# Optimization experiments

Hardware: AMD Instinct MI355X
Metric: run time of the kernel (lower is better)

Reference implementation:

```python
import jax, jax.numpy as jnp
import numpy as np

N_NODES = 100000   # n_all_trajs
N_EDGES = 640000
HIDDEN = 128
N_USERS = 1000


def gcn_conv(x, edge_index, edge_weight, W, b, num_nodes):
    """PyG GCNConv with add_self_loops=False, normalize=True.
    out[col] += (deg^-1/2[row] * w * deg^-1/2[col]) * (x @ W)[row]; then + b.
    deg is weighted in-degree at the target (col) nodes."""
    row, col = edge_index[0], edge_index[1]
    deg = jax.ops.segment_sum(edge_weight, col, num_segments=num_nodes)
    deg_inv_sqrt = jnp.where(deg > 0, jax.lax.rsqrt(jnp.maximum(deg, 1e-30)), 0.0)
    norm = deg_inv_sqrt[row] * edge_weight * deg_inv_sqrt[col]   # [E]
    h = x @ W                                                    # [N, H]
    msg = h[row] * norm[:, None]                                 # [E, H] gather+scale
    out = jax.ops.segment_sum(msg, col, num_segments=num_nodes)  # scatter-add
    return out + b


def setup_inputs() -> dict:
    key = jax.random.key(0)
    ks = jax.random.split(key, 9)
    edge_index = jax.random.randint(ks[0], (2, N_EDGES), 0, N_NODES, dtype=jnp.int64)
    edge_weight = jax.random.uniform(ks[1], (N_EDGES,), dtype=jnp.float32)
    emb = jax.random.normal(ks[2], (N_NODES, HIDDEN), dtype=jnp.float32) * 0.02
    W1 = jax.random.normal(ks[3], (HIDDEN, HIDDEN), dtype=jnp.float32) * 0.05
    b1 = jax.random.normal(ks[4], (HIDDEN,), dtype=jnp.float32) * 0.01
    W2 = jax.random.normal(ks[5], (HIDDEN, HIDDEN), dtype=jnp.float32) * 0.05
    b2 = jax.random.normal(ks[6], (HIDDEN,), dtype=jnp.float32) * 0.01
    Wp = jax.random.normal(ks[7], (HIDDEN, N_USERS), dtype=jnp.float32) * 0.05
    bp = jax.random.normal(ks[8], (N_USERS,), dtype=jnp.float32) * 0.01
    return {"edge_index": edge_index, "edge_weight": edge_weight, "emb": emb,
            "W1": W1, "b1": b1, "W2": W2, "b2": b2, "Wp": Wp, "bp": bp}


def reference(edge_index, edge_weight, emb, W1, b1, W2, b2, Wp, bp):
    h1 = gcn_conv(emb, edge_index, edge_weight, W1, b1, N_NODES)
    # dropout p=0.0 (inference) -> identity
    h2 = gcn_conv(h1, edge_index, edge_weight, W2, b2, N_NODES)
    predictions = h2 @ Wp + bp   # [N_NODES, N_USERS]
    return predictions
```

## Files before the change

kernel.cpp:

```cpp
#include <hip/hip_runtime.h>

#define N_NODES 100000
#define N_EDGES 640000
#define HIDDEN  128
#define N_USERS 1000
#define CAP     64

using u16 = unsigned short;
using u32 = unsigned int;

using short8  = __attribute__((ext_vector_type(8))) short;
using floatx4 = __attribute__((ext_vector_type(4))) float;

__device__ __forceinline__ u16 f2bf(float f) {
  u32 u = __float_as_uint(f);
  u32 r = u + 0x7FFFu + ((u >> 16) & 1u);
  return (u16)(r >> 16);
}
__device__ __forceinline__ u32 pack2bf(float a, float b) {
  return (u32)f2bf(a) | ((u32)f2bf(b) << 16);
}
__device__ __forceinline__ float bflo2f(u32 v) { return __uint_as_float(v << 16); }


__global__ void wcomb1(const float* __restrict__ W1, const float* __restrict__ b1,
                       const float* __restrict__ W2,
                       float* __restrict__ T1, float* __restrict__ t1) {
  int idx = blockIdx.x * 256 + threadIdx.x;
  if (idx >= 129 * 128) return;
  int k = idx >> 7, c = idx & 127;
  const float* src = (k < 128) ? (W1 + (size_t)k * 128) : b1;
  float s = 0.f;
  for (int j = 0; j < 128; ++j) s += src[j] * W2[(size_t)j * 128 + c];
  if (k < 128) T1[(size_t)k * 128 + c] = s;
  else         t1[c] = s;
}

__global__ void wcomb2(const float* __restrict__ T1, const float* __restrict__ Wp,
                       u16* __restrict__ WcT) {
  int idx = blockIdx.x * 256 + threadIdx.x;
  int c = idx >> 7, k = idx & 127;
  float s = 0.f;
  if (c < N_USERS)
    for (int l = 0; l < 128; ++l) s += T1[(size_t)k * 128 + l] * Wp[(size_t)l * N_USERS + c];
  WcT[idx] = f2bf(s);
}

__global__ void wcomb3(const float* __restrict__ t1, const float* __restrict__ b2,
                       const float* __restrict__ Wp, const float* __restrict__ bp,
                       float* __restrict__ u, float* __restrict__ v) {
  int idx = blockIdx.x * 256 + threadIdx.x;
  if (idx >= 2 * N_USERS) return;
  if (idx < N_USERS) {
    float s = 0.f;
    for (int j = 0; j < 128; ++j) s += t1[j] * Wp[(size_t)j * N_USERS + idx];
    u[idx] = s;
  } else {
    int c = idx - N_USERS;
    float s = bp[c];
    for (int j = 0; j < 128; ++j) s += b2[j] * Wp[(size_t)j * N_USERS + c];
    v[c] = s;
  }
}

__global__ void cast_kernel(const float* __restrict__ x, u16* __restrict__ xb, int total8) {
  int i = blockIdx.x * 256 + threadIdx.x;
  if (i >= total8) return;
  const float4* s4 = (const float4*)(x + (size_t)i * 8);
  float4 lo = s4[0], hi = s4[1];
  uint4 o;
  o.x = pack2bf(lo.x, lo.y); o.y = pack2bf(lo.z, lo.w);
  o.z = pack2bf(hi.x, hi.y); o.w = pack2bf(hi.z, hi.w);
  ((uint4*)xb)[i] = o;
}

__global__ void deg_kernel(const int* __restrict__ col, const float* __restrict__ w,
                           float* __restrict__ deg, int E) {
  int i = blockIdx.x * 256 + threadIdx.x;
  if (i < E) atomicAdd(&deg[col[i]], w[i]);
}

__global__ void dis_kernel(const float* __restrict__ deg, float* __restrict__ dis, int M) {
  int i = blockIdx.x * 256 + threadIdx.x;
  if (i < M) {
    float d = deg[i];
    dis[i] = d > 0.f ? rsqrtf(d) : 0.f;
  }
}

__global__ void bucket_kernel(const int* __restrict__ row, const int* __restrict__ col,
                              const float* __restrict__ w, const float* __restrict__ dis,
                              int* __restrict__ counts, int2* __restrict__ pairs, int E) {
  int i = blockIdx.x * 256 + threadIdx.x;
  if (i >= E) return;
  int r = row[i], c = col[i];
  int pos = atomicAdd(&counts[c], 1);
  if (pos < CAP) {
    pairs[((size_t)c << 6) + (size_t)pos] = make_int2(r, __float_as_int(dis[r] * w[i] * dis[c]));
  }
}

template<bool S1OUT>
__global__ __launch_bounds__(256)
void agg_kernel(const u16* __restrict__ hb, const int* __restrict__ counts,
                const int2* __restrict__ pairs, float* __restrict__ s1,
                u16* __restrict__ out, int M) {
  int wid  = threadIdx.x >> 6;
  int lane = threadIdx.x & 63;
  int n = blockIdx.x * 4 + wid;
  if (n >= M) return;
  int cnt = counts[n];
  cnt = cnt < CAP ? cnt : CAP;
  int2 my = make_int2(0, 0);
  if (lane < cnt) my = pairs[((size_t)n << 6) + lane];
  int   sv = my.x;
  float wv = __int_as_float(my.y);
  const u32* h32 = (const u32*)hb;
  float ax = 0.f, ay = 0.f;
  int e = 0;
  for (; e + 4 <= cnt; e += 4) {
    int   s0 = __shfl(sv, e),     s1_ = __shfl(sv, e + 1);
    int   s2 = __shfl(sv, e + 2), s3  = __shfl(sv, e + 3);
    float w0 = __shfl(wv, e),     w1  = __shfl(wv, e + 1);
    float w2 = __shfl(wv, e + 2), w3  = __shfl(wv, e + 3);
    u32 h0 = h32[((size_t)s0 << 6) + lane];
    u32 h1 = h32[((size_t)s1_ << 6) + lane];
    u32 h2 = h32[((size_t)s2 << 6) + lane];
    u32 h3 = h32[((size_t)s3 << 6) + lane];
    ax += w0 * bflo2f(h0 & 0xFFFFu); ay += w0 * __uint_as_float(h0 & 0xFFFF0000u);
    ax += w1 * bflo2f(h1 & 0xFFFFu); ay += w1 * __uint_as_float(h1 & 0xFFFF0000u);
    ax += w2 * bflo2f(h2 & 0xFFFFu); ay += w2 * __uint_as_float(h2 & 0xFFFF0000u);
    ax += w3 * bflo2f(h3 & 0xFFFFu); ay += w3 * __uint_as_float(h3 & 0xFFFF0000u);
  }
  for (; e < cnt; ++e) {
    int   s = __shfl(sv, e);
    float w = __shfl(wv, e);
    u32 hv = h32[((size_t)s << 6) + lane];
    ax += w * bflo2f(hv & 0xFFFFu);
    ay += w * __uint_as_float(hv & 0xFFFF0000u);
  }
  if (S1OUT) {
    float t = wv;
    for (int o = 32; o; o >>= 1) t += __shfl_xor(t, o);
    if (lane == 0) s1[n] = t;
  }
  u32 lo = (u32)f2bf(ax);
  u32 hi = (u32)f2bf(ay);
  ((u32*)out)[((size_t)n << 6) + lane] = lo | (hi << 16);
}

__global__ __launch_bounds__(256, 2)
void gemm_final(const u16* __restrict__ A, const u16* __restrict__ BT,
                const float* __restrict__ s1, const float* __restrict__ u,
                const float* __restrict__ vv, float* __restrict__ outf, int M) {
  __shared__ u16 As[128 * 128];
  __shared__ u16 Bs[128 * 128];
  const int m0 = (blockIdx.x >> 3) * 128;
  const int n0 = (blockIdx.x & 7) * 128;
  const int tid = threadIdx.x;

  for (int i = 0; i < 8; ++i) {
    int chunk = tid + i * 256;
    int row = chunk >> 4;
    int c   = chunk & 15;
    int sw  = ((c ^ (row & 15)) << 3);
    int gr  = m0 + row;
    uint4 av = {0u, 0u, 0u, 0u};
    if (gr < M) av = *(const uint4*)(A + ((size_t)gr << 7) + (c << 3));
    *(uint4*)(&As[(row << 7) + sw]) = av;
    uint4 bv = *(const uint4*)(BT + ((size_t)(n0 + row) << 7) + (c << 3));
    *(uint4*)(&Bs[(row << 7) + sw]) = bv;
  }
  __syncthreads();

  const int wid  = tid >> 6, lane = tid & 63;
  const int wr = (wid >> 1) << 6;
  const int wc = (wid & 1) << 6;
  const int lm = lane & 15, quad = lane >> 4;

  floatx4 acc[4][4] = {};
  for (int ks = 0; ks < 4; ++ks) {
    int cks = ks * 4 + quad;
    int sw  = ((cks ^ lm) << 3);
    short8 a[4], b[4];
    for (int i = 0; i < 4; ++i)
      a[i] = *(const short8*)(&As[((wr + i * 16 + lm) << 7) + sw]);
    for (int j = 0; j < 4; ++j)
      b[j] = *(const short8*)(&Bs[((wc + j * 16 + lm) << 7) + sw]);
    for (int i = 0; i < 4; ++i)
      for (int j = 0; j < 4; ++j)
        acc[i][j] = __builtin_amdgcn_mfma_f32_16x16x32_bf16(a[i], b[j], acc[i][j], 0, 0, 0);
  }

  for (int i = 0; i < 4; ++i) {
    int rb = m0 + wr + i * 16 + quad * 4;
    float sr[4];
    for (int r = 0; r < 4; ++r) sr[r] = (rb + r < M) ? s1[rb + r] : 0.f;
    for (int j = 0; j < 4; ++j) {
      int col = n0 + wc + j * 16 + lm;
      if (col < N_USERS) {
        float uc = u[col], vc = vv[col];
        for (int r = 0; r < 4; ++r) {
          int row = rb + r;
          if (row < M)
            outf[(size_t)row * N_USERS + col] = acc[i][j][r] + sr[r] * uc + vc;
        }
      }
    }
  }
}

extern "C" void kernel_launch(void* const* d_in, const int* in_sizes, int n_in,
                              void* d_out, int out_size, void* d_ws, size_t ws_size,
                              hipStream_t stream) {
  const int*   eidx = (const int*)d_in[0];
  const int*   erow = eidx;
  const int*   ecol = eidx + N_EDGES;
  const float* ew   = (const float*)d_in[1];
  const float* emb  = (const float*)d_in[2];
  const float* W1   = (const float*)d_in[3];
  const float* b1   = (const float*)d_in[4];
  const float* W2   = (const float*)d_in[5];
  const float* b2   = (const float*)d_in[6];
  const float* Wp   = (const float*)d_in[7];
  const float* bp   = (const float*)d_in[8];
  float* out = (float*)d_out;

  const int M = N_NODES, E = N_EDGES;

  char* p = (char*)d_ws;
  float* deg    = (float*)p;  p += 400128;
  int*   counts = (int*)p;    p += 400128;
  float* dis    = (float*)p;  p += 400128;
  int2*  pairs  = (int2*)p;   p += (size_t)M * CAP * 8;
  u16*   Xb     = (u16*)p;    p += (size_t)M * 128 * 2;
  u16*   g      = (u16*)p;    p += (size_t)M * 128 * 2;
  float* T1     = (float*)p;  p += 128 * 128 * 4;
  float* t1     = (float*)p;  p += 512;
  u16*   WcT    = (u16*)p;    p += 1024 * 128 * 2;
  float* uvec   = (float*)p;  p += 4096;
  float* vvec   = (float*)p;  p += 4096;
  float* s1     = dis;

  hipMemsetAsync(deg, 0, 400128 + 400128, stream);

  wcomb1<<<65,  256, 0, stream>>>(W1, b1, W2, T1, t1);
  wcomb2<<<512, 256, 0, stream>>>(T1, Wp, WcT);
  wcomb3<<<8,   256, 0, stream>>>(t1, b2, Wp, bp, uvec, vvec);

  cast_kernel<<<(M * 16 + 255) / 256, 256, 0, stream>>>(emb, Xb, M * 16);

  deg_kernel<<<(E + 255) / 256, 256, 0, stream>>>(ecol, ew, deg, E);
  dis_kernel<<<(M + 255) / 256, 256, 0, stream>>>(deg, dis, M);
  bucket_kernel<<<(E + 255) / 256, 256, 0, stream>>>(erow, ecol, ew, dis, counts, pairs, E);

  agg_kernel<true ><<<(M + 3) / 4, 256, 0, stream>>>(Xb, counts, pairs, s1, g, M);
  agg_kernel<false><<<(M + 3) / 4, 256, 0, stream>>>(g,  counts, pairs, nullptr, Xb, M);

  const int mt = (M + 127) / 128;
  gemm_final<<<mt * 8, 256, 0, stream>>>(Xb, WcT, s1, uvec, vvec, out, M);
}
```

Measured before the change: 790.5 us.

## Merge prep kernels into two launches, widen aggregation loads, nontemporal output stores

Folds the seven small preprocessing kernels (cast, degree, rsqrt, bucketing, weight combination) into two block-partitioned kernels, computing rsqrt of degree inline instead of in a separate pass. The aggregation kernel now has each half-wave process alternate edges with 8-byte loads, then combines the halves with a cross-lane reduction. The final GEMM epilogue hoists the u/v column loads and writes output with nontemporal stores. The aim is less launch overhead and more memory parallelism, at the cost of an extra shuffle reduction and the half-wave store idling.

```diff
diff --git a/kernel.cpp b/kernel.cpp
--- a/kernel.cpp
+++ b/kernel.cpp
@@ -23,80 +23,75 @@
 __device__ __forceinline__ float bflo2f(u32 v) { return __uint_as_float(v << 16); }
 
 
-__global__ void wcomb1(const float* __restrict__ W1, const float* __restrict__ b1,
-                       const float* __restrict__ W2,
-                       float* __restrict__ T1, float* __restrict__ t1) {
-  int idx = blockIdx.x * 256 + threadIdx.x;
-  if (idx >= 129 * 128) return;
-  int k = idx >> 7, c = idx & 127;
-  const float* src = (k < 128) ? (W1 + (size_t)k * 128) : b1;
-  float s = 0.f;
-  for (int j = 0; j < 128; ++j) s += src[j] * W2[(size_t)j * 128 + c];
-  if (k < 128) T1[(size_t)k * 128 + c] = s;
-  else         t1[c] = s;
-}
-
-__global__ void wcomb2(const float* __restrict__ T1, const float* __restrict__ Wp,
-                       u16* __restrict__ WcT) {
-  int idx = blockIdx.x * 256 + threadIdx.x;
-  int c = idx >> 7, k = idx & 127;
-  float s = 0.f;
-  if (c < N_USERS)
-    for (int l = 0; l < 128; ++l) s += T1[(size_t)k * 128 + l] * Wp[(size_t)l * N_USERS + c];
-  WcT[idx] = f2bf(s);
-}
-
-__global__ void wcomb3(const float* __restrict__ t1, const float* __restrict__ b2,
-                       const float* __restrict__ Wp, const float* __restrict__ bp,
-                       float* __restrict__ u, float* __restrict__ v) {
-  int idx = blockIdx.x * 256 + threadIdx.x;
-  if (idx >= 2 * N_USERS) return;
-  if (idx < N_USERS) {
+__global__ __launch_bounds__(256)
+void prep_kernel(const float* __restrict__ emb, u16* __restrict__ xb,
+                 const int* __restrict__ ecol, const float* __restrict__ ew,
+                 float* __restrict__ deg,
+                 const float* __restrict__ W1, const float* __restrict__ b1,
+                 const float* __restrict__ W2,
+                 float* __restrict__ T1, float* __restrict__ t1) {
+  int b = blockIdx.x;
+  if (b < 6250) {
+    int i = b * 256 + threadIdx.x;
+    const float4* s4 = (const float4*)(emb + (size_t)i * 8);
+    float4 lo = s4[0], hi = s4[1];
+    uint4 o;
+    o.x = pack2bf(lo.x, lo.y); o.y = pack2bf(lo.z, lo.w);
+    o.z = pack2bf(hi.x, hi.y); o.w = pack2bf(hi.z, hi.w);
+    ((uint4*)xb)[i] = o;
+  } else if (b < 8750) {
+    int i = (b - 6250) * 256 + threadIdx.x;
+    atomicAdd(&deg[ecol[i]], ew[i]);
+  } else {
+    int idx = (b - 8750) * 256 + threadIdx.x;
+    if (idx >= 129 * 128) return;
+    int k = idx >> 7, c = idx & 127;
+    const float* src = (k < 128) ? (W1 + (size_t)k * 128) : b1;
     float s = 0.f;
-    for (int j = 0; j < 128; ++j) s += t1[j] * Wp[(size_t)j * N_USERS + idx];
-    u[idx] = s;
+    for (int j = 0; j < 128; ++j) s += src[j] * W2[(size_t)j * 128 + c];
+    if (k < 128) T1[(size_t)k * 128 + c] = s;
+    else         t1[c] = s;
+  }
+}
+
+__global__ __launch_bounds__(256)
+void stage2_kernel(const int* __restrict__ erow, const int* __restrict__ ecol,
+                   const float* __restrict__ ew, const float* __restrict__ deg,
+                   int* __restrict__ counts, int2* __restrict__ pairs,
+                   const float* __restrict__ T1, const float* __restrict__ t1,
+                   const float* __restrict__ b2, const float* __restrict__ Wp,
+                   const float* __restrict__ bp,
+                   u16* __restrict__ WcT, float* __restrict__ u, float* __restrict__ v) {
+  int b = blockIdx.x;
+  if (b < 2500) {
+    int i = b * 256 + threadIdx.x;
+    int r = erow[i], c = ecol[i];
+    float dr = deg[r], dc = deg[c];
+    float nr = dr > 0.f ? rsqrtf(dr) : 0.f;
+    float nc = dc > 0.f ? rsqrtf(dc) : 0.f;
+    int pos = atomicAdd(&counts[c], 1);
+    if (pos < CAP)
+      pairs[((size_t)c << 6) + (size_t)pos] = make_int2(r, __float_as_int(nr * ew[i] * nc));
+  } else if (b < 3012) {
+    int idx = (b - 2500) * 256 + threadIdx.x;
+    int c = idx >> 7, k = idx & 127;
+    float s = 0.f;
+    if (c < N_USERS)
+      for (int l = 0; l < 128; ++l) s += T1[(size_t)k * 128 + l] * Wp[(size_t)l * N_USERS + c];
+    WcT[idx] = f2bf(s);
   } else {
-    int c = idx - N_USERS;
-    float s = bp[c];
-    for (int j = 0; j < 128; ++j) s += b2[j] * Wp[(size_t)j * N_USERS + c];
-    v[c] = s;
-  }
-}
-
-__global__ void cast_kernel(const float* __restrict__ x, u16* __restrict__ xb, int total8) {
-  int i = blockIdx.x * 256 + threadIdx.x;
-  if (i >= total8) return;
-  const float4* s4 = (const float4*)(x + (size_t)i * 8);
-  float4 lo = s4[0], hi = s4[1];
-  uint4 o;
-  o.x = pack2bf(lo.x, lo.y); o.y = pack2bf(lo.z, lo.w);
-  o.z = pack2bf(hi.x, hi.y); o.w = pack2bf(hi.z, hi.w);
-  ((uint4*)xb)[i] = o;
-}
-
-__global__ void deg_kernel(const int* __restrict__ col, const float* __restrict__ w,
-                           float* __restrict__ deg, int E) {
-  int i = blockIdx.x * 256 + threadIdx.x;
-  if (i < E) atomicAdd(&deg[col[i]], w[i]);
-}
-
-__global__ void dis_kernel(const float* __restrict__ deg, float* __restrict__ dis, int M) {
-  int i = blockIdx.x * 256 + threadIdx.x;
-  if (i < M) {
-    float d = deg[i];
-    dis[i] = d > 0.f ? rsqrtf(d) : 0.f;
-  }
-}
-
-__global__ void bucket_kernel(const int* __restrict__ row, const int* __restrict__ col,
-                              const float* __restrict__ w, const float* __restrict__ dis,
-                              int* __restrict__ counts, int2* __restrict__ pairs, int E) {
-  int i = blockIdx.x * 256 + threadIdx.x;
-  if (i >= E) return;
-  int r = row[i], c = col[i];
-  int pos = atomicAdd(&counts[c], 1);
-  if (pos < CAP) {
-    pairs[((size_t)c << 6) + (size_t)pos] = make_int2(r, __float_as_int(dis[r] * w[i] * dis[c]));
+    int idx = (b - 3012) * 256 + threadIdx.x;
+    if (idx >= 2 * N_USERS) return;
+    if (idx < N_USERS) {
+      float s = 0.f;
+      for (int j = 0; j < 128; ++j) s += t1[j] * Wp[(size_t)j * N_USERS + idx];
+      u[idx] = s;
+    } else {
+      int c = idx - N_USERS;
+      float s = bp[c];
+      for (int j = 0; j < 128; ++j) s += b2[j] * Wp[(size_t)j * N_USERS + c];
+      v[c] = s;
+    }
   }
 }
 
@@ -115,38 +110,43 @@
   if (lane < cnt) my = pairs[((size_t)n << 6) + lane];
   int   sv = my.x;
   float wv = __int_as_float(my.y);
-  const u32* h32 = (const u32*)hb;
-  float ax = 0.f, ay = 0.f;
-  int e = 0;
-  for (; e + 4 <= cnt; e += 4) {
-    int   s0 = __shfl(sv, e),     s1_ = __shfl(sv, e + 1);
-    int   s2 = __shfl(sv, e + 2), s3  = __shfl(sv, e + 3);
-    float w0 = __shfl(wv, e),     w1  = __shfl(wv, e + 1);
-    float w2 = __shfl(wv, e + 2), w3  = __shfl(wv, e + 3);
-    u32 h0 = h32[((size_t)s0 << 6) + lane];
-    u32 h1 = h32[((size_t)s1_ << 6) + lane];
-    u32 h2 = h32[((size_t)s2 << 6) + lane];
-    u32 h3 = h32[((size_t)s3 << 6) + lane];
-    ax += w0 * bflo2f(h0 & 0xFFFFu); ay += w0 * __uint_as_float(h0 & 0xFFFF0000u);
-    ax += w1 * bflo2f(h1 & 0xFFFFu); ay += w1 * __uint_as_float(h1 & 0xFFFF0000u);
-    ax += w2 * bflo2f(h2 & 0xFFFFu); ay += w2 * __uint_as_float(h2 & 0xFFFF0000u);
-    ax += w3 * bflo2f(h3 & 0xFFFFu); ay += w3 * __uint_as_float(h3 & 0xFFFF0000u);
-  }
-  for (; e < cnt; ++e) {
+  const uint2* h8 = (const uint2*)hb;
+  int half = lane >> 5, l5 = lane & 31;
+  float a0 = 0.f, a1 = 0.f, a2 = 0.f, a3 = 0.f;
+  int trips = (cnt + 1) >> 1;
+  int t = 0;
+  for (; t + 2 <= trips; t += 2) {
+    int e0 = 2 * t + half, e1 = 2 * t + 2 + half;
+    int   s0 = __shfl(sv, e0), s1_ = __shfl(sv, e1);
+    float w0 = __shfl(wv, e0), w1  = __shfl(wv, e1);
+    uint2 h0 = h8[((size_t)s0  << 5) + l5];
+    uint2 h1 = h8[((size_t)s1_ << 5) + l5];
+    a0 += w0 * bflo2f(h0.x & 0xFFFFu); a1 += w0 * __uint_as_float(h0.x & 0xFFFF0000u);
+    a2 += w0 * bflo2f(h0.y & 0xFFFFu); a3 += w0 * __uint_as_float(h0.y & 0xFFFF0000u);
+    a0 += w1 * bflo2f(h1.x & 0xFFFFu); a1 += w1 * __uint_as_float(h1.x & 0xFFFF0000u);
+    a2 += w1 * bflo2f(h1.y & 0xFFFFu); a3 += w1 * __uint_as_float(h1.y & 0xFFFF0000u);
+  }
+  for (; t < trips; ++t) {
+    int e = 2 * t + half;
     int   s = __shfl(sv, e);
     float w = __shfl(wv, e);
-    u32 hv = h32[((size_t)s << 6) + lane];
-    ax += w * bflo2f(hv & 0xFFFFu);
-    ay += w * __uint_as_float(hv & 0xFFFF0000u);
-  }
+    uint2 h = h8[((size_t)s << 5) + l5];
+    a0 += w * bflo2f(h.x & 0xFFFFu); a1 += w * __uint_as_float(h.x & 0xFFFF0000u);
+    a2 += w * bflo2f(h.y & 0xFFFFu); a3 += w * __uint_as_float(h.y & 0xFFFF0000u);
+  }
+  a0 += __shfl_xor(a0, 32); a1 += __shfl_xor(a1, 32);
+  a2 += __shfl_xor(a2, 32); a3 += __shfl_xor(a3, 32);
   if (S1OUT) {
-    float t = wv;
-    for (int o = 32; o; o >>= 1) t += __shfl_xor(t, o);
-    if (lane == 0) s1[n] = t;
-  }
-  u32 lo = (u32)f2bf(ax);
-  u32 hi = (u32)f2bf(ay);
-  ((u32*)out)[((size_t)n << 6) + lane] = lo | (hi << 16);
+    float tt = wv;
+    for (int o = 32; o; o >>= 1) tt += __shfl_xor(tt, o);
+    if (lane == 0) s1[n] = tt;
+  }
+  if (half == 0) {
+    uint2 o;
+    o.x = pack2bf(a0, a1);
+    o.y = pack2bf(a2, a3);
+    ((uint2*)out)[((size_t)n << 5) + l5] = o;
+  }
 }
 
 __global__ __launch_bounds__(256, 2)
@@ -192,18 +192,27 @@
         acc[i][j] = __builtin_amdgcn_mfma_f32_16x16x32_bf16(a[i], b[j], acc[i][j], 0, 0, 0);
   }
 
+  float uc[4], vc[4];
+  int   colv[4];
+  bool  ok[4];
+  for (int j = 0; j < 4; ++j) {
+    int col = n0 + wc + j * 16 + lm;
+    colv[j] = col;
+    ok[j]   = col < N_USERS;
+    uc[j]   = ok[j] ? u[col]  : 0.f;
+    vc[j]   = ok[j] ? vv[col] : 0.f;
+  }
   for (int i = 0; i < 4; ++i) {
     int rb = m0 + wr + i * 16 + quad * 4;
     float sr[4];
     for (int r = 0; r < 4; ++r) sr[r] = (rb + r < M) ? s1[rb + r] : 0.f;
     for (int j = 0; j < 4; ++j) {
-      int col = n0 + wc + j * 16 + lm;
-      if (col < N_USERS) {
-        float uc = u[col], vc = vv[col];
+      if (ok[j]) {
         for (int r = 0; r < 4; ++r) {
           int row = rb + r;
           if (row < M)
-            outf[(size_t)row * N_USERS + col] = acc[i][j][r] + sr[r] * uc + vc;
+            __builtin_nontemporal_store(acc[i][j][r] + sr[r] * uc[j] + vc[j],
+                                        &outf[(size_t)row * N_USERS + colv[j]]);
         }
       }
     }
@@ -226,12 +235,12 @@
   const float* bp   = (const float*)d_in[8];
   float* out = (float*)d_out;
 
-  const int M = N_NODES, E = N_EDGES;
+  const int M = N_NODES;
 
   char* p = (char*)d_ws;
   float* deg    = (float*)p;  p += 400128;
   int*   counts = (int*)p;    p += 400128;
-  float* dis    = (float*)p;  p += 400128;
+  float* s1     = (float*)p;  p += 400128;
   int2*  pairs  = (int2*)p;   p += (size_t)M * CAP * 8;
   u16*   Xb     = (u16*)p;    p += (size_t)M * 128 * 2;
   u16*   g      = (u16*)p;    p += (size_t)M * 128 * 2;
@@ -240,19 +249,12 @@
   u16*   WcT    = (u16*)p;    p += 1024 * 128 * 2;
   float* uvec   = (float*)p;  p += 4096;
   float* vvec   = (float*)p;  p += 4096;
-  float* s1     = dis;
 
   hipMemsetAsync(deg, 0, 400128 + 400128, stream);
 
-  wcomb1<<<65,  256, 0, stream>>>(W1, b1, W2, T1, t1);
-  wcomb2<<<512, 256, 0, stream>>>(T1, Wp, WcT);
-  wcomb3<<<8,   256, 0, stream>>>(t1, b2, Wp, bp, uvec, vvec);
-
-  cast_kernel<<<(M * 16 + 255) / 256, 256, 0, stream>>>(emb, Xb, M * 16);
-
-  deg_kernel<<<(E + 255) / 256, 256, 0, stream>>>(ecol, ew, deg, E);
-  dis_kernel<<<(M + 255) / 256, 256, 0, stream>>>(deg, dis, M);
-  bucket_kernel<<<(E + 255) / 256, 256, 0, stream>>>(erow, ecol, ew, dis, counts, pairs, E);
+  prep_kernel<<<8815, 256, 0, stream>>>(emb, Xb, ecol, ew, deg, W1, b1, W2, T1, t1);
+  stage2_kernel<<<3020, 256, 0, stream>>>(erow, ecol, ew, deg, counts, pairs,
+                                          T1, t1, b2, Wp, bp, WcT, uvec, vvec);
 
   agg_kernel<true ><<<(M + 3) / 4, 256, 0, stream>>>(Xb, counts, pairs, s1, g, M);
   agg_kernel<false><<<(M + 3) / 4, 256, 0, stream>>>(g,  counts, pairs, nullptr, Xb, M);
```

After: 816.6 us. 1.03x slower.
